# Optimization experiments

Hardware: AMD Instinct MI355X
Metric: run time of the kernel (lower is better)

## Reference

```python
import jax, jax.numpy as jnp
import numpy as np

V = 27      # vocab (26 upper chars + 1)
E = 64      # embedding dim
H = 100     # GRU hidden dim
S = 10      # sequence length
B = 32768   # batch


def setup_inputs() -> dict:
    key = jax.random.key(0)
    ks = jax.random.split(key, 10)
    s = 0.08
    return {
        "encoder_X": jax.random.randint(ks[0], (B, S), 0, V),
        "decoder_X": jax.random.randint(ks[1], (B, S), 0, V),
        "emb": jax.random.normal(ks[2], (V, E)) * s,
        "enc_Wih": jax.random.normal(ks[3], (3 * H, E)) * s,
        "enc_Whh": jax.random.normal(ks[4], (3 * H, H)) * s,
        "enc_bih": jnp.zeros((3 * H,)),
        "enc_bhh": jnp.zeros((3 * H,)),
        "dec_Wih": jax.random.normal(ks[5], (3 * H, E + H)) * s,
        "dec_Whh": jax.random.normal(ks[6], (3 * H, H)) * s,
        "dec_bih": jnp.zeros((3 * H,)),
        "dec_bhh": jnp.zeros((3 * H,)),
        "attn_W": jax.random.normal(ks[7], (H, H)) * s,
        "lin_W": jax.random.normal(ks[8], (V, H)) * s,
        "lin_b": jnp.zeros((V,)),
    }


def gru_cell(x, h, Wih, Whh, bih, bhh):
    # PyTorch GRU cell: gates ordered [reset, update, new]
    gx = x @ Wih.T + bih            # [B, 3H]
    gh = h @ Whh.T + bhh            # [B, 3H]
    xr, xz, xn = jnp.split(gx, 3, axis=-1)
    hr, hz, hn = jnp.split(gh, 3, axis=-1)
    r = jax.nn.sigmoid(xr + hr)
    z = jax.nn.sigmoid(xz + hz)
    n = jnp.tanh(xn + r * hn)
    return (1.0 - z) * n + z * h


def reference(encoder_X, decoder_X, emb, enc_Wih, enc_Whh, enc_bih, enc_bhh,
              dec_Wih, dec_Whh, dec_bih, dec_bhh, attn_W, lin_W, lin_b):
    b = encoder_X.shape[0]
    # ---- encoder ----
    enc_e = emb[encoder_X]                         # [B, S, E]
    h0 = jnp.zeros((b, H), dtype=emb.dtype)

    def enc_step(h, x_t):
        h2 = gru_cell(x_t, h, enc_Wih, enc_Whh, enc_bih, enc_bhh)
        return h2, h2

    hT, enc_seq = jax.lax.scan(enc_step, h0, jnp.swapaxes(enc_e, 0, 1))
    enc_out = jnp.swapaxes(enc_seq, 0, 1)          # [B, S, H]

    # attention_W(encoder_out) is step-invariant: precompute once
    We = enc_out @ attn_W.T                        # [B, S, H]

    # ---- decoder with per-step bilinear attention ----
    dec_e = emb[decoder_X]                         # [B, S, E]

    def dec_step(h, x_t):
        score = jnp.einsum('bsh,bh->bs', We, h)    # [B, S]
        w = jax.nn.softmax(score, axis=1)
        ctx = jnp.einsum('bs,bsh->bh', w, enc_out) # [B, H]
        inp = jnp.concatenate([x_t, ctx], axis=-1) # [B, E+H]
        h2 = gru_cell(inp, h, dec_Wih, dec_Whh, dec_bih, dec_bhh)
        return h2, h2

    _, dec_seq = jax.lax.scan(dec_step, hT, jnp.swapaxes(dec_e, 0, 1))
    dec_out = jnp.swapaxes(dec_seq, 0, 1)          # [B, S, H]

    logits = dec_out @ lin_W.T + lin_b             # [B, S, V]
    return logits.reshape(-1, V)                   # [B*S, V]
```

## Files before the change

### kernel.cpp

```cpp
#include <hip/hip_runtime.h>
#include <hip/hip_bf16.h>

typedef short s16x8 __attribute__((ext_vector_type(8)));
typedef float f32x4 __attribute__((ext_vector_type(4)));
typedef unsigned short ushort_t;
typedef unsigned int uint;

#define DEV static __device__ __forceinline__

namespace {
constexpr int kV = 27, kS = 10, kB = 32768;
constexpr int BT = 64, NB = kB / BT;

constexpr size_t O_BE_R   = 0;
constexpr size_t O_BE_Z   = O_BE_R   + (size_t)7*4*512;
constexpr size_t O_BE_NH  = O_BE_Z   + (size_t)7*4*512;
constexpr size_t O_BE_NHL = O_BE_NH  + (size_t)7*4*512;
constexpr size_t O_BE_NX  = O_BE_NHL + (size_t)7*4*512;
constexpr size_t O_BE_NXL = O_BE_NX  + (size_t)7*1*512;
constexpr size_t O_BD_R   = O_BE_NXL + (size_t)7*1*512;
constexpr size_t O_BD_Z   = O_BD_R   + (size_t)7*8*512;
constexpr size_t O_BD_NC  = O_BD_Z   + (size_t)7*8*512;
constexpr size_t O_BD_NCL = O_BD_NC  + (size_t)7*5*512;
constexpr size_t O_BD_NH  = O_BD_NCL + (size_t)7*5*512;
constexpr size_t O_BD_NHL = O_BD_NH  + (size_t)7*4*512;
constexpr size_t O_WATT   = O_BD_NHL + (size_t)7*4*512;
constexpr size_t O_BLIN   = O_WATT   + (size_t)7*4*512;
constexpr size_t O_BLINL  = O_BLIN   + (size_t)2*4*512;
}

DEV float sigm(float x) { return 1.f / (1.f + __expf(-x)); }
DEV float tanh_(float x) {
  const float ax = fabsf(x), t = __expf(-2.f * ax);
  return copysignf((1.f - t) / (1.f + t), x);
}
DEV ushort_t f2b(float f) { return __builtin_bit_cast(ushort_t, __float2bfloat16(f)); }
DEV float b2f(ushort_t u) { return __builtin_bit_cast(float, (uint)u << 16); }
DEV float lo16(uint u) { return __builtin_bit_cast(float, u << 16); }
DEV float hi16(uint u) { return __builtin_bit_cast(float, u & 0xFFFF0000u); }
DEV f32x4 MF(s16x8 a, s16x8 b, f32x4 c) {
  return __builtin_amdgcn_mfma_f32_16x16x32_bf16(a, b, c, 0, 0, 0);
}
DEV float dot64(const float* __restrict__ a, const float* __restrict__ b) {
  float s = 0.f;
#pragma unroll 16
  for (int k = 0; k < 64; ++k) s += a[k] * b[k];
  return s;
}
DEV void storeHL(ushort_t* ws, size_t offH, size_t offL, int e, float v) {
  const ushort_t h = f2b(v);
  ws[offH + e] = h;
  ws[offL + e] = f2b(v - b2f(h));
}

DEV s16x8 ldBF(const ushort_t* p, int fragIdx, int lane) {
  return __builtin_bit_cast(s16x8, *(const uint4*)(p + ((size_t)fragIdx << 9) + (lane << 3)));
}
DEV uint swzb(int row, int byteoff) { return (uint)((row * 512 + byteoff) ^ ((row & 7) << 4)); }
DEV s16x8 ldA(const ushort_t* A, int rt, int kf, int cl, int g4) {
  const int row = rt * 16 + cl;
  return __builtin_bit_cast(s16x8, *(const uint4*)((const char*)A + swzb(row, kf * 64 + g4 * 16)));
}
DEV void stA16(ushort_t* A, int row, int col, ushort_t v) {
  *(ushort_t*)((char*)A + swzb(row, col * 2)) = v;
}
DEV void stA32(ushort_t* A, int row, int byteoff, uint v) {
  *(uint*)((char*)A + swzb(row, byteoff)) = v;
}
DEV uint2 ldA64(const ushort_t* A, int row, int byteoff) {
  return *(const uint2*)((const char*)A + swzb(row, byteoff));
}

__global__ void seq2seq_setup(const float* __restrict__ emb,
    const float* __restrict__ eWih, const float* __restrict__ eWhh,
    const float* __restrict__ ebih, const float* __restrict__ ebhh,
    const float* __restrict__ dWih, const float* __restrict__ dWhh,
    const float* __restrict__ dbih, const float* __restrict__ dbhh,
    const float* __restrict__ attnW, const float* __restrict__ linW,
    const float* __restrict__ linb, ushort_t* __restrict__ ws) {
  const int t0 = blockIdx.x * blockDim.x + threadIdx.x;
  const int stp = gridDim.x * blockDim.x;

  for (int e = t0; e < 7 * 4 * 512; e += stp) {
    int c = e >> 11, rem = e & 2047, fi = rem >> 9, l = (rem >> 3) & 63, i8 = rem & 7;
    int d = 16 * c + (l & 15);
    int k = fi * 32 + ((l >> 4) << 3) + i8;
    float vr = 0, vz = 0, vnh = 0;
    if (d < 100) {
      if (k < 100) { vr = eWhh[d*100+k]; vz = eWhh[(100+d)*100+k]; vnh = eWhh[(200+d)*100+k]; }
      else if (k < 127) {
        int tok = k - 100;
        vr = dot64(emb + tok*64, eWih + (size_t)d*64);
        vz = dot64(emb + tok*64, eWih + (size_t)(100+d)*64);
      } else {
        vr = ebih[d] + ebhh[d]; vz = ebih[100+d] + ebhh[100+d]; vnh = ebhh[200+d];
      }
    }
    ws[O_BE_R + e] = f2b(vr);
    ws[O_BE_Z + e] = f2b(vz);
    storeHL(ws, O_BE_NH, O_BE_NHL, e, vnh);
  }
  for (int e = t0; e < 7 * 512; e += stp) {
    int c = e >> 9, l = (e >> 3) & 63, i8 = e & 7;
    int d = 16 * c + (l & 15);
    int k = 96 + ((l >> 4) << 3) + i8;
    float v = 0;
    if (d < 100) {
      if (k >= 100 && k < 127) v = dot64(emb + (k-100)*64, eWih + (size_t)(200+d)*64);
      else if (k == 127) v = ebih[200+d];
    }
    storeHL(ws, O_BE_NX, O_BE_NXL, e, v);
  }
  for (int e = t0; e < 7 * 8 * 512; e += stp) {
    int c = e >> 12, rem = e & 4095, fi = rem >> 9, l = (rem >> 3) & 63, i8 = rem & 7;
    int d = 16 * c + (l & 15);
    int k = fi * 32 + ((l >> 4) << 3) + i8;
    float vr = 0, vz = 0;
    if (d < 100) {
      int wr = d, wz = 100 + d;
      if (k < 100)       { vr = dWih[(size_t)wr*164+64+k]; vz = dWih[(size_t)wz*164+64+k]; }
      else if (k < 128)  { }
      else if (k < 228)  { vr = dWhh[wr*100+k-128];        vz = dWhh[wz*100+k-128]; }
      else if (k < 255)  { vr = dot64(emb+(k-228)*64, dWih+(size_t)wr*164);
                           vz = dot64(emb+(k-228)*64, dWih+(size_t)wz*164); }
      else               { vr = dbih[wr]+dbhh[wr];         vz = dbih[wz]+dbhh[wz]; }
    }
    ws[O_BD_R + e] = f2b(vr);
    ws[O_BD_Z + e] = f2b(vz);
  }
  for (int e = t0; e < 7 * 5 * 512; e += stp) {
    int c = e / (5*512), rem = e - c*5*512, fi = rem >> 9, l = (rem >> 3) & 63, i8 = rem & 7;
    int fid = (fi < 4) ? fi : 7;
    int d = 16 * c + (l & 15);
    int k = fid * 32 + ((l >> 4) << 3) + i8;
    float v = 0;
    if (d < 100) {
      int wr = 200 + d;
      if (k < 100) v = dWih[(size_t)wr*164+64+k];
      else if (k >= 228 && k < 255) v = dot64(emb+(k-228)*64, dWih+(size_t)wr*164);
      else if (k == 255) v = dbih[wr];
    }
    storeHL(ws, O_BD_NC, O_BD_NCL, e, v);
  }
  for (int e = t0; e < 7 * 4 * 512; e += stp) {
    int c = e >> 11, rem = e & 2047, fi = rem >> 9, l = (rem >> 3) & 63, i8 = rem & 7;
    int d = 16 * c + (l & 15);
    int k = (4 + fi) * 32 + ((l >> 4) << 3) + i8;
    float v = 0;
    if (d < 100) {
      int wr = 200 + d;
      if (k >= 128 && k < 228) v = dWhh[wr*100+k-128];
      else if (k == 255) v = dbhh[wr];
    }
    storeHL(ws, O_BD_NH, O_BD_NHL, e, v);
  }
  for (int e = t0; e < 7 * 4 * 512; e += stp) {
    int c = e >> 11, rem = e & 2047, fi = rem >> 9, l = (rem >> 3) & 63, i8 = rem & 7;
    int d = 16 * c + (l & 15);
    int k = (4 + fi) * 32 + ((l >> 4) << 3) + i8;
    float v = 0;
    if (d < 100 && k >= 128 && k < 228) v = attnW[(k-128)*100 + d];
    ws[O_WATT + e] = f2b(v);
  }
  for (int e = t0; e < 2 * 4 * 512; e += stp) {
    int c = e >> 11, rem = e & 2047, fi = rem >> 9, l = (rem >> 3) & 63, i8 = rem & 7;
    int vv = 16 * c + (l & 15);
    int k = (4 + fi) * 32 + ((l >> 4) << 3) + i8;
    float v = 0;
    if (vv < kV) {
      if (k >= 128 && k < 228) v = linW[vv*100 + k-128];
      else if (k == 255) v = linb[vv];
    }
    storeHL(ws, O_BLIN, O_BLINL, e, v);
  }
}

__global__ __launch_bounds__(512, 1)
void seq2seq_main(const int* __restrict__ encX, const int* __restrict__ decX,
                  const ushort_t* __restrict__ ws, float* __restrict__ out) {
  const int tid  = threadIdx.x;
  const int lane = tid & 63;
  const int w    = __builtin_amdgcn_readfirstlane(tid >> 6);
  const int cl   = lane & 15, g4 = lane >> 4;
  const int c    = w;
  const int b0   = blockIdx.x * BT;

  __shared__ alignas(16) ushort_t Ash[BT * 256];
  __shared__ alignas(16) ushort_t Esh[10 * BT * 100];
  __shared__ alignas(16) float    Ssh[BT * 10];

  const ushort_t* BER   = ws + O_BE_R;
  const ushort_t* BEZ   = ws + O_BE_Z;
  const ushort_t* BENH  = ws + O_BE_NH;
  const ushort_t* BENHL = ws + O_BE_NHL;
  const ushort_t* BENX  = ws + O_BE_NX;
  const ushort_t* BENXL = ws + O_BE_NXL;
  const ushort_t* BDR   = ws + O_BD_R;
  const ushort_t* BDZ   = ws + O_BD_Z;
  const ushort_t* BDNC  = ws + O_BD_NC;
  const ushort_t* BDNCL = ws + O_BD_NCL;
  const ushort_t* BDNH  = ws + O_BD_NH;
  const ushort_t* BDNHL = ws + O_BD_NHL;
  const ushort_t* WATT  = ws + O_WATT;
  const ushort_t* BLIN  = ws + O_BLIN;
  const ushort_t* BLINL = ws + O_BLINL;

  float hreg[4][4];
#pragma unroll
  for (int rt = 0; rt < 4; ++rt)
#pragma unroll
    for (int i = 0; i < 4; ++i) hreg[rt][i] = 0.f;

  auto onehot = [&](const int* X, int tt, int baseByte) {
    if (w < 4) {
      const int tok = X[(b0 + lane) * kS + tt];
#pragma unroll
      for (int p = 0; p < 4; ++p) {
        const int j0 = w * 8 + 2 * p;
        if (j0 <= 26) {
          const uint lo = (j0 == tok || j0 == 27) ? 0x3F80u : 0u;
          const uint hi = (j0 + 1 == tok || j0 + 1 == 27) ? 0x3F80u : 0u;
          stA32(Ash, lane, baseByte + j0 * 2, lo | (hi << 16));
        }
      }
    }
  };

  for (int i = tid; i < BT * 256 / 2; i += 512) ((uint*)Ash)[i] = 0u;
  __syncthreads();
  onehot(encX, 0, 200);
  __syncthreads();

  for (int t = 0; t < kS; ++t) {
    if (w < 7) {
      f32x4 R[4], Zx[4], NHa[4], NXa[4];
#pragma unroll
      for (int rt = 0; rt < 4; ++rt) {
        R[rt] = f32x4{0,0,0,0}; Zx[rt] = f32x4{0,0,0,0};
        NHa[rt] = f32x4{0,0,0,0}; NXa[rt] = f32x4{0,0,0,0};
      }
#pragma unroll
      for (int kf = 0; kf < 4; ++kf) {
        s16x8 a[4];
#pragma unroll
        for (int rt = 0; rt < 4; ++rt) a[rt] = ldA(Ash, rt, kf, cl, g4);
        s16x8 br  = ldBF(BER,   c * 4 + kf, lane);
        s16x8 bz  = ldBF(BEZ,   c * 4 + kf, lane);
        s16x8 bh  = ldBF(BENH,  c * 4 + kf, lane);
        s16x8 bhl = ldBF(BENHL, c * 4 + kf, lane);
#pragma unroll
        for (int rt = 0; rt < 4; ++rt) {
          R[rt]   = MF(a[rt], br, R[rt]);
          Zx[rt]  = MF(a[rt], bz, Zx[rt]);
          NHa[rt] = MF(a[rt], bh, NHa[rt]);
          NHa[rt] = MF(a[rt], bhl, NHa[rt]);
        }
        if (kf == 3) {
          s16x8 bx  = ldBF(BENX,  c, lane);
          s16x8 bxl = ldBF(BENXL, c, lane);
#pragma unroll
          for (int rt = 0; rt < 4; ++rt) {
            NXa[rt] = MF(a[rt], bx, NXa[rt]);
            NXa[rt] = MF(a[rt], bxl, NXa[rt]);
          }
        }
      }
#pragma unroll
      for (int rt = 0; rt < 4; ++rt)
#pragma unroll
        for (int i = 0; i < 4; ++i) {
          const float r = sigm(R[rt][i]);
          const float z = sigm(Zx[rt][i]);
          const float n = tanh_(NXa[rt][i] + r * NHa[rt][i]);
          hreg[rt][i] = (1.f - z) * n + z * hreg[rt][i];
        }
    }
    __syncthreads();
    if (w < 7) {
      const int d = 16 * c + cl;
      if (d < 100) {
#pragma unroll
        for (int rt = 0; rt < 4; ++rt)
#pragma unroll
          for (int i = 0; i < 4; ++i) {
            const int row = rt * 16 + g4 * 4 + i;
            const ushort_t us = f2b(hreg[rt][i]);
            Esh[t * 6400 + row * 100 + d] = us;
            stA16(Ash, row, (t < 9) ? d : 128 + d, us);
          }
      }
    }
    if (t < 9) onehot(encX, t + 1, 200);
    else       onehot(decX, 0, 456);
    __syncthreads();
  }

  for (int t = 0; t < kS; ++t) {
    if (w < 7) {
      f32x4 G[4] = {f32x4{0,0,0,0}, f32x4{0,0,0,0}, f32x4{0,0,0,0}, f32x4{0,0,0,0}};
#pragma unroll
      for (int fi = 0; fi < 4; ++fi) {
        s16x8 bg = ldBF(WATT, c * 4 + fi, lane);
#pragma unroll
        for (int rt = 0; rt < 4; ++rt)
          G[rt] = MF(ldA(Ash, rt, 4 + fi, cl, g4), bg, G[rt]);
      }
      const int d = 16 * c + cl;
      if (d < 100) {
#pragma unroll
        for (int rt = 0; rt < 4; ++rt)
#pragma unroll
          for (int i = 0; i < 4; ++i)
            stA16(Ash, rt * 16 + g4 * 4 + i, d, f2b(G[rt][i]));
      }
    }
    __syncthreads();
    {
      auto score_task = [&](int s) {
        const ushort_t* ep = Esh + s * 6400 + lane * 100;
        float acc = 0.f;
#pragma unroll
        for (int jj = 0; jj < 25; ++jj) {
          uint2 gv = ldA64(Ash, lane, jj * 8);
          uint2 ev = *(const uint2*)(ep + jj * 4);
          acc += lo16(gv.x) * lo16(ev.x) + hi16(gv.x) * hi16(ev.x)
               + lo16(gv.y) * lo16(ev.y) + hi16(gv.y) * hi16(ev.y);
        }
        Ssh[lane * 10 + s] = acc;
      };
      score_task(w);
      if (w < 2) score_task(8 + w);
    }
    __syncthreads();
    {
      float wat[10];
      {
        float sc[10];
#pragma unroll
        for (int s = 0; s < 10; ++s) sc[s] = Ssh[lane * 10 + s];
        float m = sc[0];
#pragma unroll
        for (int s = 1; s < 10; ++s) m = fmaxf(m, sc[s]);
        float sum = 0.f;
#pragma unroll
        for (int s = 0; s < 10; ++s) { wat[s] = __expf(sc[s] - m); sum += wat[s]; }
        const float inv = 1.f / sum;
#pragma unroll
        for (int s = 0; s < 10; ++s) wat[s] *= inv;
      }
      const int start = w * 12 + 2 * ((w < 2) ? w : 2);
      const int nu = (w < 2) ? 7 : 6;
#pragma unroll
      for (int u = 0; u < 7; ++u) {
        if (u < nu) {
          const int d0 = start + 2 * u;
          float v0 = 0.f, v1 = 0.f;
#pragma unroll
          for (int s = 0; s < 10; ++s) {
            const uint ev = *(const uint*)(Esh + s * 6400 + lane * 100 + d0);
            v0 += wat[s] * lo16(ev);
            v1 += wat[s] * hi16(ev);
          }
          stA32(Ash, lane, d0 * 2, (uint)f2b(v0) | ((uint)f2b(v1) << 16));
        }
      }
    }
    __syncthreads();
    if (w < 7) {
      f32x4 R[4], Zx[4], NC[4], NHa[4];
#pragma unroll
      for (int rt = 0; rt < 4; ++rt) {
        R[rt] = f32x4{0,0,0,0}; Zx[rt] = f32x4{0,0,0,0};
        NC[rt] = f32x4{0,0,0,0}; NHa[rt] = f32x4{0,0,0,0};
      }
#pragma unroll
      for (int kf = 0; kf < 8; ++kf) {
        s16x8 a[4];
#pragma unroll
        for (int rt = 0; rt < 4; ++rt) a[rt] = ldA(Ash, rt, kf, cl, g4);
        s16x8 br = ldBF(BDR, c * 8 + kf, lane);
        s16x8 bz = ldBF(BDZ, c * 8 + kf, lane);
#pragma unroll
        for (int rt = 0; rt < 4; ++rt) {
          R[rt]  = MF(a[rt], br, R[rt]);
          Zx[rt] = MF(a[rt], bz, Zx[rt]);
        }
        if (kf < 4 || kf == 7) {
          const int fi = (kf < 4) ? kf : 4;
          s16x8 bnc  = ldBF(BDNC,  c * 5 + fi, lane);
          s16x8 bncl = ldBF(BDNCL, c * 5 + fi, lane);
#pragma unroll
          for (int rt = 0; rt < 4; ++rt) {
            NC[rt] = MF(a[rt], bnc, NC[rt]);
            NC[rt] = MF(a[rt], bncl, NC[rt]);
          }
        }
        if (kf >= 4) {
          const int fi = kf - 4;
          s16x8 bnh  = ldBF(BDNH,  c * 4 + fi, lane);
          s16x8 bnhl = ldBF(BDNHL, c * 4 + fi, lane);
#pragma unroll
          for (int rt = 0; rt < 4; ++rt) {
            NHa[rt] = MF(a[rt], bnh, NHa[rt]);
            NHa[rt] = MF(a[rt], bnhl, NHa[rt]);
          }
        }
      }
#pragma unroll
      for (int rt = 0; rt < 4; ++rt)
#pragma unroll
        for (int i = 0; i < 4; ++i) {
          const float r = sigm(R[rt][i]);
          const float z = sigm(Zx[rt][i]);
          const float n = tanh_(NC[rt][i] + r * NHa[rt][i]);
          hreg[rt][i] = (1.f - z) * n + z * hreg[rt][i];
        }
    }
    __syncthreads();
    if (w < 7) {
      const int d = 16 * c + cl;
      if (d < 100) {
#pragma unroll
        for (int rt = 0; rt < 4; ++rt)
#pragma unroll
          for (int i = 0; i < 4; ++i)
            stA16(Ash, rt * 16 + g4 * 4 + i, 128 + d, f2b(hreg[rt][i]));
      }
    }
    if (t < 9) onehot(decX, t + 1, 456);
    __syncthreads();
    {
      const int rtL = w >> 1, vt = w & 1;
      f32x4 aL = f32x4{0,0,0,0};
#pragma unroll
      for (int fi = 0; fi < 4; ++fi) {
        s16x8 a = ldA(Ash, rtL, 4 + fi, cl, g4);
        aL = MF(a, ldBF(BLIN,  vt * 4 + fi, lane), aL);
        aL = MF(a, ldBF(BLINL, vt * 4 + fi, lane), aL);
      }
      const int v = vt * 16 + cl;
      if (v < kV) {
#pragma unroll
        for (int i = 0; i < 4; ++i) {
          const int row = rtL * 16 + g4 * 4 + i;
          __builtin_nontemporal_store(aL[i], &out[((size_t)(b0 + row) * kS + t) * kV + v]);
        }
      }
    }
  }
}

extern "C" void kernel_launch(void* const* d_in, const int* in_sizes, int n_in,
                              void* d_out, int out_size, void* d_ws, size_t ws_size,
                              hipStream_t stream) {
  const int*   encX = (const int*)d_in[0];
  const int*   decX = (const int*)d_in[1];
  const float* emb  = (const float*)d_in[2];
  const float* eWih = (const float*)d_in[3];
  const float* eWhh = (const float*)d_in[4];
  const float* ebih = (const float*)d_in[5];
  const float* ebhh = (const float*)d_in[6];
  const float* dWih = (const float*)d_in[7];
  const float* dWhh = (const float*)d_in[8];
  const float* dbih = (const float*)d_in[9];
  const float* dbhh = (const float*)d_in[10];
  const float* attW = (const float*)d_in[11];
  const float* linW = (const float*)d_in[12];
  const float* linb = (const float*)d_in[13];
  ushort_t* ws = (ushort_t*)d_ws;
  float* o = (float*)d_out;

  seq2seq_setup<<<128, 256, 0, stream>>>(emb, eWih, eWhh, ebih, ebhh,
                                         dWih, dWhh, dbih, dbhh, attW, linW, linb, ws);
  seq2seq_main<<<NB, 512, 0, stream>>>(encX, decX, ws, o);
}
```

Baseline: 457.4 us.

## Halve batch tile to 32 rows and remap attention work for multi-block occupancy

Shrinks the per-block batch tile from 64 to 32 rows, which halves the LDS footprint and per-thread accumulators, and raises launch bounds to allow several blocks per CU. The score and context phases are remapped to half-wave row groups, and scores are now stored in a padding slot of each encoder-state row (stride 102) instead of a separate buffer. The aim is better latency hiding in this synchronization-bound recurrent kernel. In exchange, each B fragment loaded from global memory now feeds half as many MFMAs, and twice as many blocks must be scheduled.

```diff
diff --git a/kernel.cpp b/kernel.cpp
--- a/kernel.cpp
+++ b/kernel.cpp
@@ -10,7 +10,7 @@
 
 namespace {
 constexpr int kV = 27, kS = 10, kB = 32768;
-constexpr int BT = 64, NB = kB / BT;
+constexpr int BT = 32, NB = kB / BT;
 
 constexpr size_t O_BE_R   = 0;
 constexpr size_t O_BE_Z   = O_BE_R   + (size_t)7*4*512;
@@ -27,6 +27,9 @@
 constexpr size_t O_WATT   = O_BD_NHL + (size_t)7*4*512;
 constexpr size_t O_BLIN   = O_WATT   + (size_t)7*4*512;
 constexpr size_t O_BLINL  = O_BLIN   + (size_t)2*4*512;
+
+constexpr int ESTR = 102;
+constexpr int EPL  = BT * ESTR;
 }
 
 DEV float sigm(float x) { return 1.f / (1.f + __expf(-x)); }
@@ -67,8 +70,8 @@
 DEV void stA32(ushort_t* A, int row, int byteoff, uint v) {
   *(uint*)((char*)A + swzb(row, byteoff)) = v;
 }
-DEV uint2 ldA64(const ushort_t* A, int row, int byteoff) {
-  return *(const uint2*)((const char*)A + swzb(row, byteoff));
+DEV uint ldA32(const ushort_t* A, int row, int byteoff) {
+  return *(const uint*)((const char*)A + swzb(row, byteoff));
 }
 
 __global__ void seq2seq_setup(const float* __restrict__ emb,
@@ -175,7 +178,7 @@
   }
 }
 
-__global__ __launch_bounds__(512, 1)
+__global__ __launch_bounds__(512, 4)
 void seq2seq_main(const int* __restrict__ encX, const int* __restrict__ decX,
                   const ushort_t* __restrict__ ws, float* __restrict__ out) {
   const int tid  = threadIdx.x;
@@ -186,8 +189,7 @@
   const int b0   = blockIdx.x * BT;
 
   __shared__ alignas(16) ushort_t Ash[BT * 256];
-  __shared__ alignas(16) ushort_t Esh[10 * BT * 100];
-  __shared__ alignas(16) float    Ssh[BT * 10];
+  __shared__ alignas(16) ushort_t Esh[kS * EPL];
 
   const ushort_t* BER   = ws + O_BE_R;
   const ushort_t* BEZ   = ws + O_BE_Z;
@@ -205,22 +207,23 @@
   const ushort_t* BLIN  = ws + O_BLIN;
   const ushort_t* BLINL = ws + O_BLINL;
 
-  float hreg[4][4];
-#pragma unroll
-  for (int rt = 0; rt < 4; ++rt)
+  float hreg[2][4];
+#pragma unroll
+  for (int rt = 0; rt < 2; ++rt)
 #pragma unroll
     for (int i = 0; i < 4; ++i) hreg[rt][i] = 0.f;
 
   auto onehot = [&](const int* X, int tt, int baseByte) {
-    if (w < 4) {
-      const int tok = X[(b0 + lane) * kS + tt];
+    if (tid < 128) {
+      const int row = tid & 31, grp = tid >> 5;
+      const int tok = X[(b0 + row) * kS + tt];
 #pragma unroll
       for (int p = 0; p < 4; ++p) {
-        const int j0 = w * 8 + 2 * p;
+        const int j0 = grp * 8 + 2 * p;
         if (j0 <= 26) {
           const uint lo = (j0 == tok || j0 == 27) ? 0x3F80u : 0u;
           const uint hi = (j0 + 1 == tok || j0 + 1 == 27) ? 0x3F80u : 0u;
-          stA32(Ash, lane, baseByte + j0 * 2, lo | (hi << 16));
+          stA32(Ash, row, baseByte + j0 * 2, lo | (hi << 16));
         }
       }
     }
@@ -233,23 +236,23 @@
 
   for (int t = 0; t < kS; ++t) {
     if (w < 7) {
-      f32x4 R[4], Zx[4], NHa[4], NXa[4];
-#pragma unroll
-      for (int rt = 0; rt < 4; ++rt) {
+      f32x4 R[2], Zx[2], NHa[2], NXa[2];
+#pragma unroll
+      for (int rt = 0; rt < 2; ++rt) {
         R[rt] = f32x4{0,0,0,0}; Zx[rt] = f32x4{0,0,0,0};
         NHa[rt] = f32x4{0,0,0,0}; NXa[rt] = f32x4{0,0,0,0};
       }
 #pragma unroll
       for (int kf = 0; kf < 4; ++kf) {
-        s16x8 a[4];
-#pragma unroll
-        for (int rt = 0; rt < 4; ++rt) a[rt] = ldA(Ash, rt, kf, cl, g4);
+        s16x8 a[2];
+#pragma unroll
+        for (int rt = 0; rt < 2; ++rt) a[rt] = ldA(Ash, rt, kf, cl, g4);
         s16x8 br  = ldBF(BER,   c * 4 + kf, lane);
         s16x8 bz  = ldBF(BEZ,   c * 4 + kf, lane);
         s16x8 bh  = ldBF(BENH,  c * 4 + kf, lane);
         s16x8 bhl = ldBF(BENHL, c * 4 + kf, lane);
 #pragma unroll
-        for (int rt = 0; rt < 4; ++rt) {
+        for (int rt = 0; rt < 2; ++rt) {
           R[rt]   = MF(a[rt], br, R[rt]);
           Zx[rt]  = MF(a[rt], bz, Zx[rt]);
           NHa[rt] = MF(a[rt], bh, NHa[rt]);
@@ -259,14 +262,14 @@
           s16x8 bx  = ldBF(BENX,  c, lane);
           s16x8 bxl = ldBF(BENXL, c, lane);
 #pragma unroll
-          for (int rt = 0; rt < 4; ++rt) {
+          for (int rt = 0; rt < 2; ++rt) {
             NXa[rt] = MF(a[rt], bx, NXa[rt]);
             NXa[rt] = MF(a[rt], bxl, NXa[rt]);
           }
         }
       }
 #pragma unroll
-      for (int rt = 0; rt < 4; ++rt)
+      for (int rt = 0; rt < 2; ++rt)
 #pragma unroll
         for (int i = 0; i < 4; ++i) {
           const float r = sigm(R[rt][i]);
@@ -280,12 +283,12 @@
       const int d = 16 * c + cl;
       if (d < 100) {
 #pragma unroll
-        for (int rt = 0; rt < 4; ++rt)
+        for (int rt = 0; rt < 2; ++rt)
 #pragma unroll
           for (int i = 0; i < 4; ++i) {
             const int row = rt * 16 + g4 * 4 + i;
             const ushort_t us = f2b(hreg[rt][i]);
-            Esh[t * 6400 + row * 100 + d] = us;
+            Esh[t * EPL + row * ESTR + d] = us;
             stA16(Ash, row, (t < 9) ? d : 128 + d, us);
           }
       }
@@ -297,47 +300,46 @@
 
   for (int t = 0; t < kS; ++t) {
     if (w < 7) {
-      f32x4 G[4] = {f32x4{0,0,0,0}, f32x4{0,0,0,0}, f32x4{0,0,0,0}, f32x4{0,0,0,0}};
+      f32x4 G[2] = {f32x4{0,0,0,0}, f32x4{0,0,0,0}};
 #pragma unroll
       for (int fi = 0; fi < 4; ++fi) {
         s16x8 bg = ldBF(WATT, c * 4 + fi, lane);
 #pragma unroll
-        for (int rt = 0; rt < 4; ++rt)
+        for (int rt = 0; rt < 2; ++rt)
           G[rt] = MF(ldA(Ash, rt, 4 + fi, cl, g4), bg, G[rt]);
       }
       const int d = 16 * c + cl;
       if (d < 100) {
 #pragma unroll
-        for (int rt = 0; rt < 4; ++rt)
+        for (int rt = 0; rt < 2; ++rt)
 #pragma unroll
           for (int i = 0; i < 4; ++i)
             stA16(Ash, rt * 16 + g4 * 4 + i, d, f2b(G[rt][i]));
       }
     }
     __syncthreads();
+    if (w < 5) {
+      const int s = 2 * w + (lane >> 5);
+      const int r = lane & 31;
+      const ushort_t* ep = Esh + s * EPL + r * ESTR;
+      float acc = 0.f;
+#pragma unroll
+      for (int jj = 0; jj < 50; ++jj) {
+        const uint gv = ldA32(Ash, r, jj * 4);
+        const uint ev = *(const uint*)(ep + jj * 2);
+        acc += lo16(gv) * lo16(ev) + hi16(gv) * hi16(ev);
+      }
+      *(float*)(ep + 100) = acc;
+    }
+    __syncthreads();
     {
-      auto score_task = [&](int s) {
-        const ushort_t* ep = Esh + s * 6400 + lane * 100;
-        float acc = 0.f;
-#pragma unroll
-        for (int jj = 0; jj < 25; ++jj) {
-          uint2 gv = ldA64(Ash, lane, jj * 8);
-          uint2 ev = *(const uint2*)(ep + jj * 4);
-          acc += lo16(gv.x) * lo16(ev.x) + hi16(gv.x) * hi16(ev.x)
-               + lo16(gv.y) * lo16(ev.y) + hi16(gv.y) * hi16(ev.y);
-        }
-        Ssh[lane * 10 + s] = acc;
-      };
-      score_task(w);
-      if (w < 2) score_task(8 + w);
-    }
-    __syncthreads();
-    {
+      const int r = lane & 31;
+      const int W = w * 2 + (lane >> 5);
       float wat[10];
       {
         float sc[10];
 #pragma unroll
-        for (int s = 0; s < 10; ++s) sc[s] = Ssh[lane * 10 + s];
+        for (int s = 0; s < 10; ++s) sc[s] = *(const float*)(Esh + s * EPL + r * ESTR + 100);
         float m = sc[0];
 #pragma unroll
         for (int s = 1; s < 10; ++s) m = fmaxf(m, sc[s]);
@@ -348,40 +350,38 @@
 #pragma unroll
         for (int s = 0; s < 10; ++s) wat[s] *= inv;
       }
-      const int start = w * 12 + 2 * ((w < 2) ? w : 2);
-      const int nu = (w < 2) ? 7 : 6;
-#pragma unroll
-      for (int u = 0; u < 7; ++u) {
-        if (u < nu) {
-          const int d0 = start + 2 * u;
+#pragma unroll
+      for (int u = 0; u < 4; ++u) {
+        const int j = W * 4 + u;
+        if (j < 50) {
           float v0 = 0.f, v1 = 0.f;
 #pragma unroll
           for (int s = 0; s < 10; ++s) {
-            const uint ev = *(const uint*)(Esh + s * 6400 + lane * 100 + d0);
+            const uint ev = *(const uint*)(Esh + s * EPL + r * ESTR + 2 * j);
             v0 += wat[s] * lo16(ev);
             v1 += wat[s] * hi16(ev);
           }
-          stA32(Ash, lane, d0 * 2, (uint)f2b(v0) | ((uint)f2b(v1) << 16));
+          stA32(Ash, r, 4 * j, (uint)f2b(v0) | ((uint)f2b(v1) << 16));
         }
       }
     }
     __syncthreads();
     if (w < 7) {
-      f32x4 R[4], Zx[4], NC[4], NHa[4];
-#pragma unroll
-      for (int rt = 0; rt < 4; ++rt) {
+      f32x4 R[2], Zx[2], NC[2], NHa[2];
+#pragma unroll
+      for (int rt = 0; rt < 2; ++rt) {
         R[rt] = f32x4{0,0,0,0}; Zx[rt] = f32x4{0,0,0,0};
         NC[rt] = f32x4{0,0,0,0}; NHa[rt] = f32x4{0,0,0,0};
       }
 #pragma unroll
       for (int kf = 0; kf < 8; ++kf) {
-        s16x8 a[4];
-#pragma unroll
-        for (int rt = 0; rt < 4; ++rt) a[rt] = ldA(Ash, rt, kf, cl, g4);
+        s16x8 a[2];
+#pragma unroll
+        for (int rt = 0; rt < 2; ++rt) a[rt] = ldA(Ash, rt, kf, cl, g4);
         s16x8 br = ldBF(BDR, c * 8 + kf, lane);
         s16x8 bz = ldBF(BDZ, c * 8 + kf, lane);
 #pragma unroll
-        for (int rt = 0; rt < 4; ++rt) {
+        for (int rt = 0; rt < 2; ++rt) {
           R[rt]  = MF(a[rt], br, R[rt]);
           Zx[rt] = MF(a[rt], bz, Zx[rt]);
         }
@@ -390,7 +390,7 @@
           s16x8 bnc  = ldBF(BDNC,  c * 5 + fi, lane);
           s16x8 bncl = ldBF(BDNCL, c * 5 + fi, lane);
 #pragma unroll
-          for (int rt = 0; rt < 4; ++rt) {
+          for (int rt = 0; rt < 2; ++rt) {
             NC[rt] = MF(a[rt], bnc, NC[rt]);
             NC[rt] = MF(a[rt], bncl, NC[rt]);
           }
@@ -400,14 +400,14 @@
           s16x8 bnh  = ldBF(BDNH,  c * 4 + fi, lane);
           s16x8 bnhl = ldBF(BDNHL, c * 4 + fi, lane);
 #pragma unroll
-          for (int rt = 0; rt < 4; ++rt) {
+          for (int rt = 0; rt < 2; ++rt) {
             NHa[rt] = MF(a[rt], bnh, NHa[rt]);
             NHa[rt] = MF(a[rt], bnhl, NHa[rt]);
           }
         }
       }
 #pragma unroll
-      for (int rt = 0; rt < 4; ++rt)
+      for (int rt = 0; rt < 2; ++rt)
 #pragma unroll
         for (int i = 0; i < 4; ++i) {
           const float r = sigm(R[rt][i]);
@@ -421,7 +421,7 @@
       const int d = 16 * c + cl;
       if (d < 100) {
 #pragma unroll
-        for (int rt = 0; rt < 4; ++rt)
+        for (int rt = 0; rt < 2; ++rt)
 #pragma unroll
           for (int i = 0; i < 4; ++i)
             stA16(Ash, rt * 16 + g4 * 4 + i, 128 + d, f2b(hreg[rt][i]));
@@ -429,7 +429,7 @@
     }
     if (t < 9) onehot(decX, t + 1, 456);
     __syncthreads();
-    {
+    if (w < 4) {
       const int rtL = w >> 1, vt = w & 1;
       f32x4 aL = f32x4{0,0,0,0};
 #pragma unroll
```

New measurement: 736.0 us. +60.9%, slower.
